# Optimization experiments

Measured on AMD Instinct MI355X. Metric: run time of the kernel, lower is better.

## Reference

```python
import jax, jax.numpy as jnp
import numpy as np

B, E, N, DIN, D0, D1 = 64, 4, 512, 64, 64, 32


def setup_inputs() -> dict:
    key = jax.random.key(0)
    k1, k2, k3, k4 = jax.random.split(key, 4)
    x = jax.random.normal(k1, (B, N, DIN), dtype=jnp.float32)
    adj = jax.random.uniform(k2, (B, E, N, N), dtype=jnp.float32)
    W1 = jax.random.normal(k3, (DIN, D0), dtype=jnp.float32) * 0.05
    b1 = jnp.zeros((D0,), dtype=jnp.float32)
    W2 = jax.random.normal(k4, (D0, D1), dtype=jnp.float32) * 0.05
    b2 = jnp.zeros((D1,), dtype=jnp.float32)
    return {"x": x, "adj": adj, "W1": W1, "b1": b1, "W2": W2, "b2": b2}


def reference(x, adj, W1, b1, W2, b2):
    # D = diag_embed(1 / sum(adj + eye(N), dim=3)); adj_n = D @ adj
    # sum over last dim of (adj + eye) == row-sum(adj) + 1; D @ adj == row scaling.
    inv_deg = 1.0 / (jnp.sum(adj, axis=3) + 1.0)            # [B,E,N]
    adj_n = inv_deg[..., None] * adj                         # [B,E,N,N]

    # linear1(input) is identical across edge types -> compute once.
    h0 = x @ W1 + b1                                         # [B,N,D0]
    hidden = jnp.einsum('benm,bmd->bend', adj_n, h0)         # per-edge-type aggregation
    hidden = jnp.sum(hidden, axis=1) + h0                    # sum over edge types + self-loop
    hidden = jnp.tanh(hidden)                                # dropout p=0 -> identity

    o0 = hidden @ W2 + b2                                    # [B,N,D1]
    out = jnp.einsum('benm,bmd->bend', adj_n, o0)
    out = jnp.sum(out, axis=1) + o0
    out = jnp.tanh(out)
    return out
```

## Files before the change

### kernel.cpp

```cpp
#include <hip/hip_runtime.h>

#define BATCH 64
#define NE    4
#define NN    512
#define DIN   64
#define D0    64
#define D1    32

__global__ __launch_bounds__(256) void k_h0(const float* __restrict__ x,
                                            const float* __restrict__ W1,
                                            const float* __restrict__ b1,
                                            float* __restrict__ h0) {
  __shared__ float W1s[DIN][D0];
  __shared__ float xs[4][DIN];
  int t = threadIdx.x;
  #pragma unroll
  for (int i = 0; i < 4; ++i) {
    int idx = t + i * 256;
    reinterpret_cast<float4*>(&W1s[0][0])[idx] = reinterpret_cast<const float4*>(W1)[idx];
  }
  int row0 = blockIdx.x * 4;
  int r = t >> 6, c = t & 63;
  xs[r][c] = x[(size_t)(row0 + r) * DIN + c];
  __syncthreads();
  float acc = b1[c];
  #pragma unroll
  for (int k = 0; k < DIN; ++k) acc += xs[r][k] * W1s[k][c];
  h0[(size_t)(row0 + r) * D0 + c] = acc;
}

__global__ __launch_bounds__(256) void k_build_A(const float* __restrict__ adj,
                                                 float* __restrict__ A) {
  int t = threadIdx.x;
  int lane = t & 63;
  int wave = t >> 6;
  int idx = blockIdx.x * 4 + wave;
  const size_t estride = (size_t)NN * NN;
  const float* base = adj + (size_t)(idx >> 9) * NE * estride + (size_t)(idx & 511) * NN;
  float4 v[NE][2];
  float inv[NE];
  #pragma unroll
  for (int e = 0; e < NE; ++e) {
    const float4* p = reinterpret_cast<const float4*>(base + e * estride);
    v[e][0] = p[lane];
    v[e][1] = p[lane + 64];
    float s = v[e][0].x + v[e][0].y + v[e][0].z + v[e][0].w
            + v[e][1].x + v[e][1].y + v[e][1].z + v[e][1].w;
    #pragma unroll
    for (int off = 32; off; off >>= 1) s += __shfl_xor(s, off);
    inv[e] = 1.0f / (s + 1.0f);
  }
  float4 vo[2];
  float* po = reinterpret_cast<float*>(vo);
  #pragma unroll
  for (int j = 0; j < 8; ++j) po[j] = 0.0f;
  #pragma unroll
  for (int e = 0; e < NE; ++e) {
    const float* pv = reinterpret_cast<const float*>(&v[e][0]);
    #pragma unroll
    for (int j = 0; j < 8; ++j) po[j] += inv[e] * pv[j];
  }
  float4* out = reinterpret_cast<float4*>(A + (size_t)idx * NN);
  out[lane]      = vo[0];
  out[lane + 64] = vo[1];
}

__global__ __launch_bounds__(256) void k_layer1(const float* __restrict__ A,
                                                const float* __restrict__ h0,
                                                const float* __restrict__ W2,
                                                const float* __restrict__ b2,
                                                float* __restrict__ o0) {
  __shared__ float As[32][68];
  __shared__ float Bs[32][D0];
  __shared__ float Hs[64][D0];
  __shared__ float W2s[D0][D1];
  int t = threadIdx.x;
  int bb = blockIdx.x >> 3;
  int rt = blockIdx.x & 7;
  int brow = rt * 64;
  {
    reinterpret_cast<float4*>(&W2s[0][0])[t]       = reinterpret_cast<const float4*>(W2)[t];
    reinterpret_cast<float4*>(&W2s[0][0])[t + 256] = reinterpret_cast<const float4*>(W2)[t + 256];
  }
  int tx = t & 15, ty = t >> 4;
  float acc[4][4] = {};
  const float* Ab = A  + ((size_t)bb * NN + brow) * NN;
  const float* Hb = h0 + (size_t)bb * NN * D0;
  int lrow = t >> 2, lkq = t & 3;
  int bk = t >> 3, bcq = t & 7;

  for (int kt = 0; kt < 16; ++kt) {
    int k0 = kt * 32;
    float4 a0 = *reinterpret_cast<const float4*>(Ab + (size_t)lrow * NN + k0 + lkq * 4);
    float4 a1 = *reinterpret_cast<const float4*>(Ab + (size_t)lrow * NN + k0 + 16 + lkq * 4);
    float4 b0 = *reinterpret_cast<const float4*>(Hb + (size_t)(k0 + bk) * D0 + bcq * 4);
    float4 b1v = *reinterpret_cast<const float4*>(Hb + (size_t)(k0 + bk) * D0 + 32 + bcq * 4);
    __syncthreads();
    {
      const float* pa0 = reinterpret_cast<const float*>(&a0);
      const float* pa1 = reinterpret_cast<const float*>(&a1);
      #pragma unroll
      for (int j = 0; j < 4; ++j) {
        As[lkq * 4 + j][lrow]      = pa0[j];
        As[16 + lkq * 4 + j][lrow] = pa1[j];
      }
      *reinterpret_cast<float4*>(&Bs[bk][bcq * 4])      = b0;
      *reinterpret_cast<float4*>(&Bs[bk][32 + bcq * 4]) = b1v;
    }
    __syncthreads();
    #pragma unroll
    for (int k = 0; k < 32; ++k) {
      float4 av = *reinterpret_cast<const float4*>(&As[k][ty * 4]);
      float4 bv = *reinterpret_cast<const float4*>(&Bs[k][tx * 4]);
      float a_[4] = {av.x, av.y, av.z, av.w};
      float b_[4] = {bv.x, bv.y, bv.z, bv.w};
      #pragma unroll
      for (int i = 0; i < 4; ++i)
        #pragma unroll
        for (int j = 0; j < 4; ++j) acc[i][j] += a_[i] * b_[j];
    }
  }
  __syncthreads();
  #pragma unroll
  for (int i = 0; i < 4; ++i) {
    int row = ty * 4 + i;
    float4 hv = *reinterpret_cast<const float4*>(Hb + (size_t)(brow + row) * D0 + tx * 4);
    Hs[row][tx * 4 + 0] = tanhf(acc[i][0] + hv.x);
    Hs[row][tx * 4 + 1] = tanhf(acc[i][1] + hv.y);
    Hs[row][tx * 4 + 2] = tanhf(acc[i][2] + hv.z);
    Hs[row][tx * 4 + 3] = tanhf(acc[i][3] + hv.w);
  }
  __syncthreads();
  int col = t & 31, r0 = (t >> 5) * 8;
  float bias = b2[col];
  for (int r = r0; r < r0 + 8; ++r) {
    float s = bias;
    #pragma unroll
    for (int k = 0; k < D0; ++k) s += Hs[r][k] * W2s[k][col];
    o0[((size_t)bb * NN + brow + r) * D1 + col] = s;
  }
}

__global__ __launch_bounds__(256) void k_layer2(const float* __restrict__ A,
                                                const float* __restrict__ o0,
                                                float* __restrict__ out) {
  __shared__ float As[32][68];
  __shared__ float Bs[32][D1];
  int t = threadIdx.x;
  int bb = blockIdx.x >> 3, rt = blockIdx.x & 7, brow = rt * 64;
  int tx = t & 15, ty = t >> 4;
  float acc[4][2] = {};
  const float* Ab = A  + ((size_t)bb * NN + brow) * NN;
  const float* Ob = o0 + (size_t)bb * NN * D1;
  int lrow = t >> 2, lkq = t & 3;
  int bk = t >> 3, bcq = t & 7;

  for (int kt = 0; kt < 16; ++kt) {
    int k0 = kt * 32;
    float4 a0 = *reinterpret_cast<const float4*>(Ab + (size_t)lrow * NN + k0 + lkq * 4);
    float4 a1 = *reinterpret_cast<const float4*>(Ab + (size_t)lrow * NN + k0 + 16 + lkq * 4);
    float4 bv = *reinterpret_cast<const float4*>(Ob + (size_t)(k0 + bk) * D1 + bcq * 4);
    __syncthreads();
    {
      const float* pa0 = reinterpret_cast<const float*>(&a0);
      const float* pa1 = reinterpret_cast<const float*>(&a1);
      #pragma unroll
      for (int j = 0; j < 4; ++j) {
        As[lkq * 4 + j][lrow]      = pa0[j];
        As[16 + lkq * 4 + j][lrow] = pa1[j];
      }
      *reinterpret_cast<float4*>(&Bs[bk][bcq * 4]) = bv;
    }
    __syncthreads();
    #pragma unroll
    for (int k = 0; k < 32; ++k) {
      float4 av = *reinterpret_cast<const float4*>(&As[k][ty * 4]);
      float2 b2v = *reinterpret_cast<const float2*>(&Bs[k][tx * 2]);
      float a_[4] = {av.x, av.y, av.z, av.w};
      #pragma unroll
      for (int i = 0; i < 4; ++i) {
        acc[i][0] += a_[i] * b2v.x;
        acc[i][1] += a_[i] * b2v.y;
      }
    }
  }
  #pragma unroll
  for (int i = 0; i < 4; ++i) {
    int row = brow + ty * 4 + i;
    float2 self = *reinterpret_cast<const float2*>(Ob + (size_t)row * D1 + tx * 2);
    float2 r;
    r.x = tanhf(acc[i][0] + self.x);
    r.y = tanhf(acc[i][1] + self.y);
    *reinterpret_cast<float2*>(out + ((size_t)bb * NN + row) * D1 + tx * 2) = r;
  }
}

extern "C" void kernel_launch(void* const* d_in, const int* in_sizes, int n_in,
                              void* d_out, int out_size, void* d_ws, size_t ws_size,
                              hipStream_t stream) {
  const float* x   = (const float*)d_in[0];
  const float* adj = (const float*)d_in[1];
  const float* W1  = (const float*)d_in[2];
  const float* b1  = (const float*)d_in[3];
  const float* W2  = (const float*)d_in[4];
  const float* b2  = (const float*)d_in[5];
  float* out = (float*)d_out;

  char* ws = (char*)d_ws;
  float* A  = (float*)ws;
  float* h0 = (float*)(ws + (size_t)67108864);
  float* o0 = (float*)(ws + (size_t)67108864 + 8388608);

  k_h0     <<<BATCH * NN / 4, 256, 0, stream>>>(x, W1, b1, h0);
  k_build_A<<<BATCH * NN / 4, 256, 0, stream>>>(adj, A);
  k_layer1 <<<BATCH * 8,      256, 0, stream>>>(A, h0, W2, b2, o0);
  k_layer2 <<<BATCH * 8,      256, 0, stream>>>(A, o0, out);
}
```

Before: 460.1 us.

## Store normalized adjacency in bf16 and use MFMA for both aggregation layers

New measurement: 409.9 us. 1.12x faster.

```diff
diff --git a/kernel.cpp b/kernel.cpp
--- a/kernel.cpp
+++ b/kernel.cpp
@@ -3,34 +3,72 @@
 #define BATCH 64
 #define NE    4
 #define NN    512
-#define DIN   64
-#define D0    64
-#define D1    32
+
+typedef __attribute__((ext_vector_type(4))) float f32x4;
+typedef __attribute__((ext_vector_type(8))) short s16x8;
+typedef __attribute__((ext_vector_type(8))) unsigned short u16x8;
+
+__device__ __forceinline__ unsigned short f2bf(float f) {
+  unsigned u = __builtin_bit_cast(unsigned, f);
+  u += 0x7fffu + ((u >> 16) & 1u);
+  return (unsigned short)(u >> 16);
+}
 
 __global__ __launch_bounds__(256) void k_h0(const float* __restrict__ x,
                                             const float* __restrict__ W1,
                                             const float* __restrict__ b1,
-                                            float* __restrict__ h0) {
-  __shared__ float W1s[DIN][D0];
-  __shared__ float xs[4][DIN];
-  int t = threadIdx.x;
+                                            float* __restrict__ h0,
+                                            unsigned short* __restrict__ h0T) {
+  __shared__ float W1s[64][68];
+  __shared__ float xs[64][68];
+  __shared__ float Ts[64][68];
+  int t = threadIdx.x;
+  int b = blockIdx.x >> 3;
+  int mt = (blockIdx.x & 7) * 64;
   #pragma unroll
   for (int i = 0; i < 4; ++i) {
-    int idx = t + i * 256;
-    reinterpret_cast<float4*>(&W1s[0][0])[idx] = reinterpret_cast<const float4*>(W1)[idx];
-  }
-  int row0 = blockIdx.x * 4;
-  int r = t >> 6, c = t & 63;
-  xs[r][c] = x[(size_t)(row0 + r) * DIN + c];
-  __syncthreads();
-  float acc = b1[c];
-  #pragma unroll
-  for (int k = 0; k < DIN; ++k) acc += xs[r][k] * W1s[k][c];
-  h0[(size_t)(row0 + r) * D0 + c] = acc;
+    int idx = i * 256 + t;
+    int k = idx >> 4, cq = idx & 15;
+    *reinterpret_cast<float4*>(&W1s[k][cq * 4]) = reinterpret_cast<const float4*>(W1)[idx];
+  }
+  const float* xb = x + ((size_t)b * NN + mt) * 64;
+  #pragma unroll
+  for (int i = 0; i < 4; ++i) {
+    int idx = i * 256 + t;
+    int m = idx >> 4, cq = idx & 15;
+    *reinterpret_cast<float4*>(&xs[m][cq * 4]) = reinterpret_cast<const float4*>(xb)[idx];
+  }
+  __syncthreads();
+  int c = t & 63, rg = t >> 6;
+  float acc[16];
+  float bias = b1[c];
+  #pragma unroll
+  for (int i = 0; i < 16; ++i) acc[i] = bias;
+  for (int k = 0; k < 64; ++k) {
+    float w = W1s[k][c];
+    #pragma unroll
+    for (int i = 0; i < 16; ++i) acc[i] += xs[rg * 16 + i][k] * w;
+  }
+  float* h0b = h0 + ((size_t)b * NN + mt) * 64;
+  #pragma unroll
+  for (int i = 0; i < 16; ++i) {
+    h0b[(size_t)(rg * 16 + i) * 64 + c] = acc[i];
+    Ts[c][rg * 16 + i] = acc[i];
+  }
+  __syncthreads();
+  int d = t >> 2, mq = t & 3;
+  unsigned short* dst = h0T + ((size_t)b * 64 + d) * NN + mt + mq * 16;
+  u16x8 oa, ob;
+  #pragma unroll
+  for (int j = 0; j < 8; ++j) oa[j] = f2bf(Ts[d][mq * 16 + j]);
+  #pragma unroll
+  for (int j = 0; j < 8; ++j) ob[j] = f2bf(Ts[d][mq * 16 + 8 + j]);
+  *reinterpret_cast<u16x8*>(dst) = oa;
+  *reinterpret_cast<u16x8*>(dst + 8) = ob;
 }
 
 __global__ __launch_bounds__(256) void k_build_A(const float* __restrict__ adj,
-                                                 float* __restrict__ A) {
+                                                 unsigned short* __restrict__ A) {
   int t = threadIdx.x;
   int lane = t & 63;
   int wave = t >> 6;
@@ -42,156 +80,142 @@
   #pragma unroll
   for (int e = 0; e < NE; ++e) {
     const float4* p = reinterpret_cast<const float4*>(base + e * estride);
-    v[e][0] = p[lane];
-    v[e][1] = p[lane + 64];
+    v[e][0] = p[lane * 2];
+    v[e][1] = p[lane * 2 + 1];
     float s = v[e][0].x + v[e][0].y + v[e][0].z + v[e][0].w
             + v[e][1].x + v[e][1].y + v[e][1].z + v[e][1].w;
     #pragma unroll
     for (int off = 32; off; off >>= 1) s += __shfl_xor(s, off);
     inv[e] = 1.0f / (s + 1.0f);
   }
-  float4 vo[2];
-  float* po = reinterpret_cast<float*>(vo);
-  #pragma unroll
-  for (int j = 0; j < 8; ++j) po[j] = 0.0f;
+  float po[8] = {0, 0, 0, 0, 0, 0, 0, 0};
   #pragma unroll
   for (int e = 0; e < NE; ++e) {
     const float* pv = reinterpret_cast<const float*>(&v[e][0]);
     #pragma unroll
     for (int j = 0; j < 8; ++j) po[j] += inv[e] * pv[j];
   }
-  float4* out = reinterpret_cast<float4*>(A + (size_t)idx * NN);
-  out[lane]      = vo[0];
-  out[lane + 64] = vo[1];
-}
-
-__global__ __launch_bounds__(256) void k_layer1(const float* __restrict__ A,
+  u16x8 ob;
+  #pragma unroll
+  for (int j = 0; j < 8; ++j) ob[j] = f2bf(po[j]);
+  *reinterpret_cast<u16x8*>(A + (size_t)idx * NN + lane * 8) = ob;
+}
+
+__global__ __launch_bounds__(256) void k_layer1(const unsigned short* __restrict__ A,
+                                                const unsigned short* __restrict__ h0T,
                                                 const float* __restrict__ h0,
                                                 const float* __restrict__ W2,
                                                 const float* __restrict__ b2,
-                                                float* __restrict__ o0) {
-  __shared__ float As[32][68];
-  __shared__ float Bs[32][D0];
-  __shared__ float Hs[64][D0];
-  __shared__ float W2s[D0][D1];
-  int t = threadIdx.x;
-  int bb = blockIdx.x >> 3;
-  int rt = blockIdx.x & 7;
-  int brow = rt * 64;
+                                                float* __restrict__ o0,
+                                                unsigned short* __restrict__ o0T) {
+  __shared__ unsigned short LT[64][520];
+  __shared__ unsigned short Hs[64][72];
+  __shared__ unsigned short W2T[32][72];
+  int t = threadIdx.x;
+  int b = blockIdx.x >> 3;
+  int brow = (blockIdx.x & 7) * 64;
+  const u16x8* src = reinterpret_cast<const u16x8*>(h0T + (size_t)b * 64 * NN);
+  #pragma unroll
+  for (int i = 0; i < 16; ++i) {
+    int idx = i * 256 + t;
+    int d = idx >> 6, ch = idx & 63;
+    *reinterpret_cast<u16x8*>(&LT[d][ch * 8]) = src[idx];
+  }
   {
-    reinterpret_cast<float4*>(&W2s[0][0])[t]       = reinterpret_cast<const float4*>(W2)[t];
-    reinterpret_cast<float4*>(&W2s[0][0])[t + 256] = reinterpret_cast<const float4*>(W2)[t + 256];
-  }
-  int tx = t & 15, ty = t >> 4;
-  float acc[4][4] = {};
-  const float* Ab = A  + ((size_t)bb * NN + brow) * NN;
-  const float* Hb = h0 + (size_t)bb * NN * D0;
-  int lrow = t >> 2, lkq = t & 3;
-  int bk = t >> 3, bcq = t & 7;
-
-  for (int kt = 0; kt < 16; ++kt) {
-    int k0 = kt * 32;
-    float4 a0 = *reinterpret_cast<const float4*>(Ab + (size_t)lrow * NN + k0 + lkq * 4);
-    float4 a1 = *reinterpret_cast<const float4*>(Ab + (size_t)lrow * NN + k0 + 16 + lkq * 4);
-    float4 b0 = *reinterpret_cast<const float4*>(Hb + (size_t)(k0 + bk) * D0 + bcq * 4);
-    float4 b1v = *reinterpret_cast<const float4*>(Hb + (size_t)(k0 + bk) * D0 + 32 + bcq * 4);
-    __syncthreads();
-    {
-      const float* pa0 = reinterpret_cast<const float*>(&a0);
-      const float* pa1 = reinterpret_cast<const float*>(&a1);
-      #pragma unroll
-      for (int j = 0; j < 4; ++j) {
-        As[lkq * 4 + j][lrow]      = pa0[j];
-        As[16 + lkq * 4 + j][lrow] = pa1[j];
-      }
-      *reinterpret_cast<float4*>(&Bs[bk][bcq * 4])      = b0;
-      *reinterpret_cast<float4*>(&Bs[bk][32 + bcq * 4]) = b1v;
-    }
-    __syncthreads();
-    #pragma unroll
-    for (int k = 0; k < 32; ++k) {
-      float4 av = *reinterpret_cast<const float4*>(&As[k][ty * 4]);
-      float4 bv = *reinterpret_cast<const float4*>(&Bs[k][tx * 4]);
-      float a_[4] = {av.x, av.y, av.z, av.w};
-      float b_[4] = {bv.x, bv.y, bv.z, bv.w};
-      #pragma unroll
-      for (int i = 0; i < 4; ++i)
-        #pragma unroll
-        for (int j = 0; j < 4; ++j) acc[i][j] += a_[i] * b_[j];
-    }
-  }
-  __syncthreads();
-  #pragma unroll
-  for (int i = 0; i < 4; ++i) {
-    int row = ty * 4 + i;
-    float4 hv = *reinterpret_cast<const float4*>(Hb + (size_t)(brow + row) * D0 + tx * 4);
-    Hs[row][tx * 4 + 0] = tanhf(acc[i][0] + hv.x);
-    Hs[row][tx * 4 + 1] = tanhf(acc[i][1] + hv.y);
-    Hs[row][tx * 4 + 2] = tanhf(acc[i][2] + hv.z);
-    Hs[row][tx * 4 + 3] = tanhf(acc[i][3] + hv.w);
-  }
-  __syncthreads();
-  int col = t & 31, r0 = (t >> 5) * 8;
-  float bias = b2[col];
-  for (int r = r0; r < r0 + 8; ++r) {
-    float s = bias;
-    #pragma unroll
-    for (int k = 0; k < D0; ++k) s += Hs[r][k] * W2s[k][col];
-    o0[((size_t)bb * NN + brow + r) * D1 + col] = s;
-  }
-}
-
-__global__ __launch_bounds__(256) void k_layer2(const float* __restrict__ A,
+    int d0 = t >> 2, d1b = (t & 3) * 8;
+    #pragma unroll
+    for (int j = 0; j < 8; ++j)
+      W2T[d1b + j][d0] = f2bf(W2[(size_t)d0 * 32 + d1b + j]);
+  }
+  __syncthreads();
+  int lane = t & 63, w = t >> 6;
+  int cl = lane & 15, g = lane >> 4;
+  int wrow = w * 16;
+  const unsigned short* Ab = A + ((size_t)b * NN + brow + wrow + cl) * NN;
+  f32x4 acc[4] = {};
+  for (int ks = 0; ks < 16; ++ks) {
+    s16x8 af = *reinterpret_cast<const s16x8*>(Ab + ks * 32 + g * 8);
+    #pragma unroll
+    for (int n = 0; n < 4; ++n) {
+      s16x8 bf = *reinterpret_cast<const s16x8*>(&LT[n * 16 + cl][ks * 32 + g * 8]);
+      acc[n] = __builtin_amdgcn_mfma_f32_16x16x32_bf16(af, bf, acc[n], 0, 0, 0);
+    }
+  }
+  const float* h0r = h0 + ((size_t)b * NN + brow + wrow) * 64;
+  #pragma unroll
+  for (int n = 0; n < 4; ++n) {
+    #pragma unroll
+    for (int q = 0; q < 4; ++q) {
+      int row = g * 4 + q;
+      float hv = h0r[(size_t)row * 64 + n * 16 + cl];
+      Hs[wrow + row][n * 16 + cl] = f2bf(tanhf(acc[n][q] + hv));
+    }
+  }
+  __syncthreads();
+  f32x4 acc2[2] = {};
+  #pragma unroll
+  for (int ks = 0; ks < 2; ++ks) {
+    s16x8 hf = *reinterpret_cast<const s16x8*>(&Hs[wrow + cl][ks * 32 + g * 8]);
+    #pragma unroll
+    for (int n = 0; n < 2; ++n) {
+      s16x8 wf = *reinterpret_cast<const s16x8*>(&W2T[n * 16 + cl][ks * 32 + g * 8]);
+      acc2[n] = __builtin_amdgcn_mfma_f32_16x16x32_bf16(hf, wf, acc2[n], 0, 0, 0);
+    }
+  }
+  float* o0r = o0 + ((size_t)b * NN + brow + wrow) * 32;
+  unsigned short* oTb = o0T + (size_t)b * 32 * NN + (brow + wrow);
+  #pragma unroll
+  for (int n = 0; n < 2; ++n) {
+    float bias = b2[n * 16 + cl];
+    #pragma unroll
+    for (int q = 0; q < 4; ++q) {
+      int row = g * 4 + q;
+      float val = acc2[n][q] + bias;
+      o0r[(size_t)row * 32 + n * 16 + cl] = val;
+      oTb[(size_t)(n * 16 + cl) * NN + row] = f2bf(val);
+    }
+  }
+}
+
+__global__ __launch_bounds__(256) void k_layer2(const unsigned short* __restrict__ A,
+                                                const unsigned short* __restrict__ o0T,
                                                 const float* __restrict__ o0,
                                                 float* __restrict__ out) {
-  __shared__ float As[32][68];
-  __shared__ float Bs[32][D1];
-  int t = threadIdx.x;
-  int bb = blockIdx.x >> 3, rt = blockIdx.x & 7, brow = rt * 64;
-  int tx = t & 15, ty = t >> 4;
-  float acc[4][2] = {};
-  const float* Ab = A  + ((size_t)bb * NN + brow) * NN;
-  const float* Ob = o0 + (size_t)bb * NN * D1;
-  int lrow = t >> 2, lkq = t & 3;
-  int bk = t >> 3, bcq = t & 7;
-
-  for (int kt = 0; kt < 16; ++kt) {
-    int k0 = kt * 32;
-    float4 a0 = *reinterpret_cast<const float4*>(Ab + (size_t)lrow * NN + k0 + lkq * 4);
-    float4 a1 = *reinterpret_cast<const float4*>(Ab + (size_t)lrow * NN + k0 + 16 + lkq * 4);
-    float4 bv = *reinterpret_cast<const float4*>(Ob + (size_t)(k0 + bk) * D1 + bcq * 4);
-    __syncthreads();
-    {
-      const float* pa0 = reinterpret_cast<const float*>(&a0);
-      const float* pa1 = reinterpret_cast<const float*>(&a1);
-      #pragma unroll
-      for (int j = 0; j < 4; ++j) {
-        As[lkq * 4 + j][lrow]      = pa0[j];
-        As[16 + lkq * 4 + j][lrow] = pa1[j];
-      }
-      *reinterpret_cast<float4*>(&Bs[bk][bcq * 4]) = bv;
-    }
-    __syncthreads();
-    #pragma unroll
-    for (int k = 0; k < 32; ++k) {
-      float4 av = *reinterpret_cast<const float4*>(&As[k][ty * 4]);
-      float2 b2v = *reinterpret_cast<const float2*>(&Bs[k][tx * 2]);
-      float a_[4] = {av.x, av.y, av.z, av.w};
-      #pragma unroll
-      for (int i = 0; i < 4; ++i) {
-        acc[i][0] += a_[i] * b2v.x;
-        acc[i][1] += a_[i] * b2v.y;
-      }
-    }
-  }
-  #pragma unroll
-  for (int i = 0; i < 4; ++i) {
-    int row = brow + ty * 4 + i;
-    float2 self = *reinterpret_cast<const float2*>(Ob + (size_t)row * D1 + tx * 2);
-    float2 r;
-    r.x = tanhf(acc[i][0] + self.x);
-    r.y = tanhf(acc[i][1] + self.y);
-    *reinterpret_cast<float2*>(out + ((size_t)bb * NN + row) * D1 + tx * 2) = r;
+  __shared__ unsigned short OT[32][520];
+  int t = threadIdx.x;
+  int b = blockIdx.x >> 3;
+  int brow = (blockIdx.x & 7) * 64;
+  const u16x8* src = reinterpret_cast<const u16x8*>(o0T + (size_t)b * 32 * NN);
+  #pragma unroll
+  for (int i = 0; i < 8; ++i) {
+    int idx = i * 256 + t;
+    int d = idx >> 6, ch = idx & 63;
+    *reinterpret_cast<u16x8*>(&OT[d][ch * 8]) = src[idx];
+  }
+  __syncthreads();
+  int lane = t & 63, w = t >> 6;
+  int cl = lane & 15, g = lane >> 4;
+  int wrow = w * 16;
+  const unsigned short* Ab = A + ((size_t)b * NN + brow + wrow + cl) * NN;
+  f32x4 acc[2] = {};
+  for (int ks = 0; ks < 16; ++ks) {
+    s16x8 af = *reinterpret_cast<const s16x8*>(Ab + ks * 32 + g * 8);
+    #pragma unroll
+    for (int n = 0; n < 2; ++n) {
+      s16x8 bf = *reinterpret_cast<const s16x8*>(&OT[n * 16 + cl][ks * 32 + g * 8]);
+      acc[n] = __builtin_amdgcn_mfma_f32_16x16x32_bf16(af, bf, acc[n], 0, 0, 0);
+    }
+  }
+  const float* o0r = o0 + ((size_t)b * NN + brow + wrow) * 32;
+  float* outr = out + ((size_t)b * NN + brow + wrow) * 32;
+  #pragma unroll
+  for (int n = 0; n < 2; ++n) {
+    #pragma unroll
+    for (int q = 0; q < 4; ++q) {
+      int row = g * 4 + q;
+      float self = o0r[(size_t)row * 32 + n * 16 + cl];
+      outr[(size_t)row * 32 + n * 16 + cl] = tanhf(acc[n][q] + self);
+    }
   }
 }
 
@@ -207,12 +231,14 @@
   float* out = (float*)d_out;
 
   char* ws = (char*)d_ws;
-  float* A  = (float*)ws;
-  float* h0 = (float*)(ws + (size_t)67108864);
-  float* o0 = (float*)(ws + (size_t)67108864 + 8388608);
-
-  k_h0     <<<BATCH * NN / 4, 256, 0, stream>>>(x, W1, b1, h0);
+  unsigned short* A   = (unsigned short*)ws;
+  float*          h0  = (float*)(ws + 33554432);
+  unsigned short* h0T = (unsigned short*)(ws + 33554432 + 8388608);
+  float*          o0  = (float*)(ws + 46137344);
+  unsigned short* o0T = (unsigned short*)(ws + 50331648);
+
+  k_h0     <<<BATCH * 8,      256, 0, stream>>>(x, W1, b1, h0, h0T);
   k_build_A<<<BATCH * NN / 4, 256, 0, stream>>>(adj, A);
-  k_layer1 <<<BATCH * 8,      256, 0, stream>>>(A, h0, W2, b2, o0);
-  k_layer2 <<<BATCH * 8,      256, 0, stream>>>(A, o0, out);
-}
+  k_layer1 <<<BATCH * 8,      256, 0, stream>>>(A, h0T, h0, W2, b2, o0, o0T);
+  k_layer2 <<<BATCH * 8,      256, 0, stream>>>(A, o0T, o0, out);
+}
```
